# Performance work log

Measured on AMD Instinct MI355X. Metric: run time of the kernel, lower is better.

The kernel has to match this reference:

```python
import jax, jax.numpy as jnp
import numpy as np

NUM_HEADS = 12
EPS = 1e-6


def rms_norm(x, w):
    # torch nn.RMSNorm: x / sqrt(mean(x^2) + eps) * w, over last dim
    var = jnp.mean(jnp.square(x), axis=-1, keepdims=True)
    return x * jax.lax.rsqrt(var + EPS) * w


def rope2d_freqs(H, W, head_dim, dtype=jnp.float32):
    dim_x = head_dim // 2
    dim_y = head_dim - dim_x
    inv_freq_x = 1.0 / (10000.0 ** (jnp.arange(0, dim_x, 2, dtype=dtype) / dim_x))  # [dim_x//2]
    inv_freq_y = 1.0 / (10000.0 ** (jnp.arange(0, dim_y, 2, dtype=dtype) / dim_y))
    seq_x = jnp.arange(W, dtype=dtype)
    seq_y = jnp.arange(H, dtype=dtype)
    freqs_x = seq_x[:, None] * inv_freq_x[None, :]            # [W, dim_x//2]
    freqs_y = seq_y[:, None] * inv_freq_y[None, :]            # [H, dim_y//2]
    emb_x = jnp.concatenate([freqs_x, freqs_x], axis=-1)      # [W, dim_x]
    emb_y = jnp.concatenate([freqs_y, freqs_y], axis=-1)      # [H, dim_y]
    emb_x = jnp.broadcast_to(emb_x[None, :, :], (H, W, dim_x))
    emb_y = jnp.broadcast_to(emb_y[:, None, :], (H, W, dim_y))
    freqs = jnp.concatenate([emb_x, emb_y], axis=-1).reshape(H * W, head_dim)
    return freqs[None, :, :]  # [1, H*W, head_dim]


def rotate_half(x):
    x1, x2 = jnp.split(x, 2, axis=-1)
    return jnp.concatenate([-x2, x1], axis=-1)


def apply_rope(q, k, freqs):
    cos = jnp.cos(freqs)
    sin = jnp.sin(freqs)
    return q * cos + rotate_half(q) * sin, k * cos + rotate_half(k) * sin


def setup_inputs() -> dict:
    key = jax.random.key(0)
    ks = jax.random.split(key, 4)
    B, H, W, C = 16, 32, 32, 768
    N = 1 + H * W
    x = jax.random.normal(ks[0], (B, N, C), dtype=jnp.float32)
    qkv_w = jax.random.normal(ks[1], (C, 3 * C), dtype=jnp.float32) * (C ** -0.5)
    proj_w = jax.random.normal(ks[2], (C, C), dtype=jnp.float32) * (C ** -0.5)
    proj_b = jax.random.normal(ks[3], (C,), dtype=jnp.float32) * 0.01
    q_norm_w = jnp.ones((C // NUM_HEADS,), dtype=jnp.float32)
    k_norm_w = jnp.ones((C // NUM_HEADS,), dtype=jnp.float32)
    return {"x": x, "qkv_w": qkv_w, "proj_w": proj_w, "proj_b": proj_b,
            "q_norm_w": q_norm_w, "k_norm_w": k_norm_w, "H": H, "W": W}


def reference(x, qkv_w, proj_w, proj_b, q_norm_w, k_norm_w, H, W):
    B, N, C = x.shape
    h = NUM_HEADS
    d = C // h
    qkv = (x @ qkv_w).reshape(B, N, 3, h, d)
    qkv = jnp.transpose(qkv, (2, 0, 3, 1, 4))  # [3, B, h, N, d]
    q, k, v = qkv[0], qkv[1], qkv[2]
    q = rms_norm(q, q_norm_w)
    k = rms_norm(k, k_norm_w)
    cls_q, q = q[:, :, :1], q[:, :, 1:]
    cls_k, k = k[:, :, :1], k[:, :, 1:]
    freqs = rope2d_freqs(H, W, d, dtype=x.dtype)  # [1, H*W, d]
    q, k = apply_rope(q, k, freqs)
    q = jnp.concatenate([cls_q, q], axis=2)
    k = jnp.concatenate([cls_k, k], axis=2)
    scale = d ** -0.5
    scores = jnp.einsum('bhqd,bhkd->bhqk', q, k) * scale
    attn = jax.nn.softmax(scores, axis=-1)
    out = jnp.einsum('bhqk,bhkd->bhqd', attn, v)  # [B, h, N, d]
    out = jnp.transpose(out, (0, 2, 1, 3)).reshape(B, N, C)
    return out @ proj_w + proj_b
```

## Files before the change

kernel.cpp:

```cpp
#include <hip/hip_runtime.h>
#include <math.h>

#define NHEADS 12
#define HD 64
#define BB 16
#define NN 1025
#define CC 768
#define MM (BB * NN)
#define QSZ ((size_t)BB * NHEADS * NN * HD)
#define NNP 1032
#define VTSZ ((size_t)BB * NHEADS * HD * NNP)

typedef __attribute__((ext_vector_type(8))) short short8;
typedef __attribute__((ext_vector_type(4))) float f32x4;
typedef __attribute__((ext_vector_type(4))) unsigned short us4;
typedef __attribute__((ext_vector_type(4))) unsigned int u32x4;
typedef unsigned short us;

typedef __attribute__((address_space(3))) unsigned int lds_u32;
typedef const __attribute__((address_space(1))) unsigned int g_u32;

__device__ __forceinline__ void gload16(const void* g, void* l) {
    __builtin_amdgcn_global_load_lds((g_u32*)g, (lds_u32*)l, 16, 0, 0);
}

__device__ __forceinline__ int imin(int a, int b) { return a < b ? a : b; }

__device__ __forceinline__ us f2h(float f) {
    _Float16 h = (_Float16)f;
    return __builtin_bit_cast(unsigned short, h);
}
__device__ __forceinline__ float h2f(us b) {
    return (float)__builtin_bit_cast(_Float16, b);
}
__device__ __forceinline__ unsigned pkrtz(float a, float b) {
    return __builtin_bit_cast(unsigned, __builtin_amdgcn_cvt_pkrtz(a, b));
}

__global__ __launch_bounds__(256) void split_x(const float* __restrict__ src,
                                               us* __restrict__ xc) {
    size_t e = ((size_t)blockIdx.x * 256 + threadIdx.x) * 8;
    float4 a = *(const float4*)(src + e);
    float4 b = *(const float4*)(src + e + 4);
    float v[8] = {a.x, a.y, a.z, a.w, b.x, b.y, b.z, b.w};
    short8 h;
#pragma unroll
    for (int j = 0; j < 8; ++j) h[j] = (short)f2h(v[j]);
    *(short8*)(xc + e) = h;
}

__global__ __launch_bounds__(256) void tsplit(const float* __restrict__ w,
                                              us* __restrict__ wc, int N) {
    __shared__ float tile[64][65];
    const int t = threadIdx.x;
    const int n0 = blockIdx.x * 64, k0 = blockIdx.y * 64;
    {
        int kr = t & 63, so = t >> 6;
#pragma unroll
        for (int g = 0; g < 4; ++g) {
            int c = (so * 4 + g) * 4;
            float4 v = *(const float4*)(w + (size_t)(k0 + kr) * N + n0 + c);
            tile[kr][c + 0] = v.x; tile[kr][c + 1] = v.y;
            tile[kr][c + 2] = v.z; tile[kr][c + 3] = v.w;
        }
    }
    __syncthreads();
    int nr = t & 63, half = t >> 6;
    short8 h0, h1;
#pragma unroll
    for (int j = 0; j < 8; ++j) h0[j] = (short)f2h(tile[half * 16 + j][nr]);
#pragma unroll
    for (int j = 0; j < 8; ++j) h1[j] = (short)f2h(tile[half * 16 + 8 + j][nr]);
    size_t o = (size_t)(n0 + nr) * CC + k0 + half * 16;
    *(short8*)(wc + o)     = h0;
    *(short8*)(wc + o + 8) = h1;
}

template<int MODE>
__global__ __launch_bounds__(512) void gemm_mfma(
    const us* __restrict__ A,
    const us* __restrict__ B,
    us* __restrict__ Q, us* __restrict__ K, us* __restrict__ Vth,
    const float* __restrict__ qnw, const float* __restrict__ knw,
    float* __restrict__ fout, const float* __restrict__ bias) {
    __shared__ __align__(16) char lds[49152];
    char* ldsA = lds;
    char* ldsB = lds + 16384;
    const int tid = threadIdx.x;
    const int lane = tid & 63, wv = tid >> 6;
    const int wn = wv >> 2, wm = wv & 3;
    const int g = lane >> 4;

    const int gx = gridDim.x;
    const int nwg = gx * gridDim.y;
    const int lin = blockIdx.y * gx + blockIdx.x;
    const int qq = nwg >> 3, rr = nwg & 7;
    const int xcd = lin & 7, idx = lin >> 3;
    const int wgid = (xcd < rr ? xcd * (qq + 1) : rr * (qq + 1) + (xcd - rr) * qq) + idx;
    const int n0 = (wgid % gx) * 128, m0 = (wgid / gx) * 256;

    f32x4 acc[4][4];
    const f32x4 fz = {0.f, 0.f, 0.f, 0.f};
#pragma unroll
    for (int a = 0; a < 4; ++a)
#pragma unroll
        for (int b = 0; b < 4; ++b) acc[a][b] = fz;

    const int srow = (wv << 3) + (lane >> 3);
    const int cb   = (lane & 7) ^ ((lane >> 3) & 7);
    size_t aoff[2], boff[4];
#pragma unroll
    for (int i = 0; i < 2; ++i)
        aoff[i] = (size_t)(n0 + i * 64 + srow) * CC + cb * 8;
#pragma unroll
    for (int i = 0; i < 4; ++i)
        boff[i] = (size_t)imin(m0 + i * 64 + srow, MM - 1) * CC + cb * 8;
    const int wdst = wv * 1024;

    for (int t = 0; t < CC / 64; ++t) {
#pragma unroll
        for (int i = 0; i < 2; ++i)
            gload16(A + aoff[i] + t * 64, ldsA + i * 8192 + wdst);
#pragma unroll
        for (int i = 0; i < 4; ++i)
            gload16(B + boff[i] + t * 64, ldsB + i * 8192 + wdst);
        __syncthreads();

        const int j  = lane >> 4;
        const int rl = lane & 15;
#pragma unroll
        for (int kh = 0; kh < 2; ++kh) {
            short8 af[4];
#pragma unroll
            for (int nc = 0; nc < 4; ++nc) {
                int ra = wn * 64 + nc * 16 + rl;
                af[nc] = *(const short8*)(ldsA + ra * 128 + ((((kh << 2) + j) ^ (ra & 7)) << 4));
            }
            __builtin_amdgcn_s_setprio(1);
#pragma unroll
            for (int mc = 0; mc < 4; ++mc) {
                int rb = wm * 64 + mc * 16 + rl;
                short8 bf = *(const short8*)(ldsB + rb * 128 + ((((kh << 2) + j) ^ (rb & 7)) << 4));
#pragma unroll
                for (int nc = 0; nc < 4; ++nc)
                    acc[nc][mc] = __builtin_amdgcn_mfma_f32_16x16x32_f16(af[nc], bf, acc[nc][mc], 0, 0, 0);
            }
            __builtin_amdgcn_s_setprio(0);
        }
        __syncthreads();
    }

    if (MODE == 0) {
        const int s = n0 / CC;
        if (s < 2) {
            float2* lut = (float2*)lds;
            {
                int pos = tid >> 4, jj = tid & 15;
                float ang = (float)pos * exp2f((float)jj * (-13.287712379549449f / 16.0f));
                lut[tid] = make_float2(cosf(ang), sinf(ang));
            }
            __syncthreads();
            const float* wvec = (s == 0) ? qnw : knw;
            float wr[4][4];
#pragma unroll
            for (int nc = 0; nc < 4; ++nc)
#pragma unroll
                for (int r = 0; r < 4; ++r) wr[nc][r] = wvec[nc * 16 + g * 4 + r];
            const float qscale = (s == 0) ? 0.125f * 1.4426950408889634f : 1.0f;
            const int head = (n0 - s * CC + wn * 64) >> 6;
            us* dst = (s == 0) ? Q : K;

#pragma unroll
            for (int mc = 0; mc < 4; ++mc) {
                int m = m0 + wm * 64 + mc * 16 + (lane & 15);
                if (m >= MM) continue;
                int b = m / NN, t = m - b * NN;
                float v[4][4];
#pragma unroll
                for (int nc = 0; nc < 4; ++nc)
#pragma unroll
                    for (int r = 0; r < 4; ++r) v[nc][r] = acc[nc][mc][r];
                float ss = 0.f;
#pragma unroll
                for (int nc = 0; nc < 4; ++nc)
#pragma unroll
                    for (int r = 0; r < 4; ++r) ss += v[nc][r] * v[nc][r];
                ss += __shfl_xor(ss, 16);
                ss += __shfl_xor(ss, 32);
                float rn = 1.0f / sqrtf(ss * (1.0f / 64.0f) + 1e-6f);
#pragma unroll
                for (int nc = 0; nc < 4; ++nc)
#pragma unroll
                    for (int r = 0; r < 4; ++r) v[nc][r] *= rn * wr[nc][r];
                if (t > 0) {
                    int px = (t - 1) & 31, py = (t - 1) >> 5;
#pragma unroll
                    for (int r = 0; r < 4; ++r) {
                        float2 ex = lut[px * 16 + g * 4 + r];
                        float2 ey = lut[py * 16 + g * 4 + r];
                        float n0v = v[0][r] * ex.x - v[2][r] * ex.y;
                        float n1v = v[1][r] * ex.x - v[3][r] * ex.y;
                        float n2v = v[2][r] * ey.x + v[0][r] * ey.y;
                        float n3v = v[3][r] * ey.x + v[1][r] * ey.y;
                        v[0][r] = n0v; v[1][r] = n1v; v[2][r] = n2v; v[3][r] = n3v;
                    }
                }
                int bh = b * NHEADS + head;
                size_t rbase = ((size_t)bh * NN + t) * HD;
#pragma unroll
                for (int nc = 0; nc < 4; ++nc) {
                    us4 h4;
#pragma unroll
                    for (int r = 0; r < 4; ++r) h4[r] = f2h(v[nc][r] * qscale);
                    *(us4*)(dst + rbase + nc * 16 + g * 4) = h4;
                }
            }
        } else {
#pragma unroll
            for (int mc = 0; mc < 4; ++mc) {
                int m = m0 + wm * 64 + mc * 16 + (lane & 15);
                if (m >= MM) continue;
                int b = m / NN, t = m - b * NN;
#pragma unroll
                for (int nc = 0; nc < 4; ++nc) {
                    int nin = (n0 - 2 * CC) + wn * 64 + nc * 16 + g * 4;
                    int head = nin >> 6;
                    int dd = nin & 63;
                    int bh = b * NHEADS + head;
#pragma unroll
                    for (int r = 0; r < 4; ++r) {
                        size_t idx2 = ((size_t)bh * HD + dd + r) * NNP + t;
                        Vth[idx2] = f2h(acc[nc][mc][r]);
                        if (t == NN - 1) {
#pragma unroll
                            for (int tt = 1; tt <= 7; ++tt) Vth[idx2 + tt] = 0;
                        }
                    }
                }
            }
        }
    } else {
#pragma unroll
        for (int mc = 0; mc < 4; ++mc) {
            int m = m0 + wm * 64 + mc * 16 + (lane & 15);
            if (m >= MM) continue;
#pragma unroll
            for (int nc = 0; nc < 4; ++nc) {
                int n = n0 + wn * 64 + nc * 16 + (g << 2);
                float4 o = {acc[nc][mc][0] + bias[n + 0], acc[nc][mc][1] + bias[n + 1],
                            acc[nc][mc][2] + bias[n + 2], acc[nc][mc][3] + bias[n + 3]};
                *(float4*)(fout + (size_t)m * CC + n) = o;
            }
        }
    }
}

__global__ __launch_bounds__(256, 4) void attn_mfma(
    const us* __restrict__ Q, const us* __restrict__ K,
    const us* __restrict__ Vth, us* __restrict__ OC) {
    __shared__ __align__(16) char smem[36864];
    const int tid = threadIdx.x;
    const int lane = tid & 63, wv = tid >> 6;
    const int g = lane >> 4, qi = lane & 15;

    int lin = blockIdx.x;
    int xcd = lin & 7, loc = lin >> 3;
    int bh  = (loc / 9) * 8 + xcd;
    int qb  = loc - (loc / 9) * 9;
    const int q0 = qb * 128;

    const size_t kbase0 = (size_t)bh * NN * HD;
    const size_t vbase0 = (size_t)bh * HD * NNP;

    short8 qf[2][2];
#pragma unroll
    for (int h = 0; h < 2; ++h) {
        int qr = imin(q0 + (wv << 5) + (h << 4) + qi, NN - 1);
        const us* qp = Q + kbase0 + (size_t)qr * HD + (g << 3);
        qf[h][0] = *(const short8*)(qp);
        qf[h][1] = *(const short8*)(qp + 32);
    }

    f32x4 oa[2][5];
    const f32x4 fz = {0.f, 0.f, 0.f, 0.f};
#pragma unroll
    for (int h = 0; h < 2; ++h)
#pragma unroll
        for (int db = 0; db < 5; ++db) oa[h][db] = fz;

    const int VB = 8192;

    *(uint2*)(smem + VB + 8192 + tid * 8) = (uint2){0x3C003C00u, 0x3C003C00u};
    *(uint2*)(smem + 18432 + VB + 8192 + tid * 8) = (uint2){0x3C003C00u, 0x3C003C00u};

    int rbase[2];
#pragma unroll
    for (int ks = 0; ks < 2; ++ks)
        rbase[ks] = qi * 128 + (((ks << 6) + (g << 4)) ^ ((qi & 7) << 4));

    const int srow = (wv << 4) + (lane >> 3);
    const int sg   = lane & 7;
    int kwoff[2], vwoff[2];
#pragma unroll
    for (int i = 0; i < 2; ++i) {
        int row = srow + (i << 3);
        int pp = ((row >> 5) << 5) | (((row >> 2) & 1) << 4) |
                 (((row >> 3) & 3) << 2) | (row & 3);
        kwoff[i] = pp * 128 + ((sg << 4) ^ ((pp & 7) << 4));
        vwoff[i] = VB + row * 128 + ((sg << 4) ^ ((row & 7) << 4));
    }

    const us* kp = K   + kbase0 + (size_t)srow * HD  + (sg << 3);
    const us* vp = Vth + vbase0 + (size_t)srow * NNP + (sg << 3);
    short8 pkh[2], pvh[2];
    pkh[0] = *(const short8*)kp;
    pkh[1] = *(const short8*)(kp + 8 * HD);
    pvh[0] = *(const short8*)vp;
    pvh[1] = *(const short8*)(vp + 8 * NNP);
    kp += 64 * HD; vp += 64;

    auto step = [&](int t, char* buf) {
        *(short8*)(buf + kwoff[0]) = pkh[0];
        *(short8*)(buf + kwoff[1]) = pkh[1];
        *(short8*)(buf + vwoff[0]) = pvh[0];
        *(short8*)(buf + vwoff[1]) = pvh[1];
        __syncthreads();
        if (t < 16) {
            pkh[0] = *(const short8*)kp;
            pkh[1] = *(const short8*)(kp + 8 * HD);
            pvh[0] = *(const short8*)vp;
            pvh[1] = *(const short8*)(vp + 8 * NNP);
            kp += 64 * HD; vp += 64;
        }
        const int j0 = t * 64;

        short8 pa[2][2];
#pragma unroll
        for (int h = 0; h < 2; ++h) {
            f32x4 sc[4];
#pragma unroll
            for (int c = 0; c < 4; ++c) sc[c] = fz;
            __builtin_amdgcn_s_setprio(1);
#pragma unroll
            for (int ks = 0; ks < 2; ++ks)
#pragma unroll
                for (int c = 0; c < 4; ++c) {
                    short8 kfh = *(const short8*)(buf + rbase[ks] + c * 2048);
                    sc[c] = __builtin_amdgcn_mfma_f32_16x16x32_f16(kfh, qf[h][ks], sc[c], 0, 0, 0);
                }
            __builtin_amdgcn_s_setprio(0);

            if (j0 + 64 > NN) {
#pragma unroll
                for (int c = 0; c < 4; ++c)
#pragma unroll
                    for (int r = 0; r < 4; ++r)
                        if (j0 + ((c >> 1) << 5) + (g << 3) + ((c & 1) << 2) + r >= NN)
                            sc[c][r] = -1e30f;
            }
#pragma unroll
            for (int ks = 0; ks < 2; ++ks) {
                u32x4 w;
                w[0] = pkrtz(exp2f(sc[2 * ks][0]), exp2f(sc[2 * ks][1]));
                w[1] = pkrtz(exp2f(sc[2 * ks][2]), exp2f(sc[2 * ks][3]));
                w[2] = pkrtz(exp2f(sc[2 * ks + 1][0]), exp2f(sc[2 * ks + 1][1]));
                w[3] = pkrtz(exp2f(sc[2 * ks + 1][2]), exp2f(sc[2 * ks + 1][3]));
                pa[h][ks] = __builtin_bit_cast(short8, w);
            }
        }

        __builtin_amdgcn_s_setprio(1);
#pragma unroll
        for (int ks = 0; ks < 2; ++ks)
#pragma unroll
            for (int db = 0; db < 5; ++db) {
                short8 vfh = *(const short8*)(buf + VB + rbase[ks] + db * 2048);
                oa[0][db] = __builtin_amdgcn_mfma_f32_16x16x32_f16(pa[0][ks], vfh, oa[0][db], 0, 0, 0);
                oa[1][db] = __builtin_amdgcn_mfma_f32_16x16x32_f16(pa[1][ks], vfh, oa[1][db], 0, 0, 0);
            }
        __builtin_amdgcn_s_setprio(0);
    };

#pragma unroll 1
    for (int tt = 0; tt < 8; ++tt) {
        step(2 * tt,     smem);
        step(2 * tt + 1, smem + 18432);
    }
    step(16, smem);

    const int b = bh / NHEADS, hh = bh - b * NHEADS;
#pragma unroll
    for (int h = 0; h < 2; ++h)
#pragma unroll
        for (int r = 0; r < 4; ++r) {
            int q = q0 + (wv << 5) + (h << 4) + (g << 2) + r;
            float linv = 1.0f / oa[h][4][r];
            if (q < NN) {
#pragma unroll
                for (int db = 0; db < 4; ++db) {
                    int d = (db << 4) + qi;
                    OC[(size_t)(b * NN + q) * CC + hh * HD + d] = f2h(oa[h][db][r] * linv);
                }
            }
        }
}

extern "C" void kernel_launch(void* const* d_in, const int* in_sizes, int n_in,
                              void* d_out, int out_size, void* d_ws, size_t ws_size,
                              hipStream_t stream) {
    const float* x      = (const float*)d_in[0];
    const float* qkv_w  = (const float*)d_in[1];
    const float* proj_w = (const float*)d_in[2];
    const float* proj_b = (const float*)d_in[3];
    const float* qnw    = (const float*)d_in[4];
    const float* knw    = (const float*)d_in[5];

    us* p = (us*)d_ws;
    us* Q   = p;                 p += QSZ;
    us* K   = p;                 p += QSZ;
    us* Vth = p;                 p += VTSZ;
    us* XC  = p;                 p += (size_t)MM * CC;
    us* WC  = p;                 p += (size_t)3 * CC * CC;
    us* PC  = p;                 p += (size_t)CC * CC;

    split_x<<<dim3((int)(((size_t)MM * CC) / 8 / 256)), 256, 0, stream>>>(x, XC);
    tsplit<<<dim3(3 * CC / 64, CC / 64), 256, 0, stream>>>(qkv_w, WC, 3 * CC);
    tsplit<<<dim3(CC / 64, CC / 64), 256, 0, stream>>>(proj_w, PC, CC);

    gemm_mfma<0><<<dim3(18, (MM + 255) / 256), 512, 0, stream>>>(
        WC, XC, Q, K, Vth, qnw, knw, nullptr, nullptr);
    attn_mfma<<<dim3(8 * 216), 256, 0, stream>>>(Q, K, Vth, XC);
    gemm_mfma<1><<<dim3(6, (MM + 255) / 256), 512, 0, stream>>>(
        PC, XC, nullptr, nullptr, nullptr, nullptr, nullptr,
        (float*)d_out, proj_b);
}
```

Baseline: 224.4 us.

## Stage attention K/V tiles via direct global-to-LDS loads with source-side swizzle

The attention kernel stops prefetching K/V tiles into registers and writing them to LDS. It now issues global_load_lds 16-byte loads straight into the next double buffer, and permutes the global source addresses so the LDS layout keeps the existing swizzled read pattern. The QK^T MFMAs for both query halves are interleaved so each loaded K fragment is used twice. The barrier moves to the end of each step, and the launch-bounds occupancy hint of 4 is dropped. The aim is to save VGPRs and LDS-store instructions and to overlap the copy with compute. The risks are correct wait-count handling before the barrier and a different register and occupancy outcome.

Measured after the change: 228.3 us. Within noise of the previous version (+1.7%).

```diff
diff --git a/kernel.cpp b/kernel.cpp
--- a/kernel.cpp
+++ b/kernel.cpp
@@ -255,7 +255,7 @@
     }
 }
 
-__global__ __launch_bounds__(256, 4) void attn_mfma(
+__global__ __launch_bounds__(256) void attn_mfma(
     const us* __restrict__ Q, const us* __restrict__ K,
     const us* __restrict__ Vth, us* __restrict__ OC) {
     __shared__ __align__(16) char smem[36864];
@@ -289,85 +289,85 @@
         for (int db = 0; db < 5; ++db) oa[h][db] = fz;
 
     const int VB = 8192;
+    const int BUFS = 18432;
 
     *(uint2*)(smem + VB + 8192 + tid * 8) = (uint2){0x3C003C00u, 0x3C003C00u};
-    *(uint2*)(smem + 18432 + VB + 8192 + tid * 8) = (uint2){0x3C003C00u, 0x3C003C00u};
+    *(uint2*)(smem + BUFS + VB + 8192 + tid * 8) = (uint2){0x3C003C00u, 0x3C003C00u};
 
     int rbase[2];
 #pragma unroll
     for (int ks = 0; ks < 2; ++ks)
         rbase[ks] = qi * 128 + (((ks << 6) + (g << 4)) ^ ((qi & 7) << 4));
 
-    const int srow = (wv << 4) + (lane >> 3);
-    const int sg   = lane & 7;
-    int kwoff[2], vwoff[2];
+    const int lrow = lane >> 3, lslot = lane & 7;
+    const us* ks_[2];
+    const us* vs_[2];
 #pragma unroll
     for (int i = 0; i < 2; ++i) {
-        int row = srow + (i << 3);
-        int pp = ((row >> 5) << 5) | (((row >> 2) & 1) << 4) |
-                 (((row >> 3) & 3) << 2) | (row & 3);
-        kwoff[i] = pp * 128 + ((sg << 4) ^ ((pp & 7) << 4));
-        vwoff[i] = VB + row * 128 + ((sg << 4) ^ ((row & 7) << 4));
-    }
-
-    const us* kp = K   + kbase0 + (size_t)srow * HD  + (sg << 3);
-    const us* vp = Vth + vbase0 + (size_t)srow * NNP + (sg << 3);
-    short8 pkh[2], pvh[2];
-    pkh[0] = *(const short8*)kp;
-    pkh[1] = *(const short8*)(kp + 8 * HD);
-    pvh[0] = *(const short8*)vp;
-    pvh[1] = *(const short8*)(vp + 8 * NNP);
-    kp += 64 * HD; vp += 64;
-
-    auto step = [&](int t, char* buf) {
-        *(short8*)(buf + kwoff[0]) = pkh[0];
-        *(short8*)(buf + kwoff[1]) = pkh[1];
-        *(short8*)(buf + vwoff[0]) = pvh[0];
-        *(short8*)(buf + vwoff[1]) = pvh[1];
-        __syncthreads();
-        if (t < 16) {
-            pkh[0] = *(const short8*)kp;
-            pkh[1] = *(const short8*)(kp + 8 * HD);
-            pvh[0] = *(const short8*)vp;
-            pvh[1] = *(const short8*)(vp + 8 * NNP);
-            kp += 64 * HD; vp += 64;
+        int pp  = (wv << 4) + (i << 3) + lrow;
+        int sig = ((pp >> 5) << 5) | (((pp >> 3) & 1) << 4) |
+                  (((pp >> 2) & 1) << 3) | (((pp >> 4) & 1) << 2) | (pp & 3);
+        ks_[i] = K + kbase0 + (size_t)sig * HD + ((lslot ^ (pp & 7)) << 3);
+        vs_[i] = Vth + vbase0 + (size_t)pp * NNP + ((lslot ^ lrow) << 3);
+    }
+    const int kd0 = wv * 2048, kd1 = wv * 2048 + 1024;
+
+    gload16(ks_[0], smem + kd0);
+    gload16(ks_[1], smem + kd1);
+    gload16(vs_[0], smem + VB + kd0);
+    gload16(vs_[1], smem + VB + kd1);
+    ks_[0] += 64 * HD; ks_[1] += 64 * HD; vs_[0] += 64; vs_[1] += 64;
+    __syncthreads();
+
+    auto step = [&](int t, char* buf, char* bufn, bool stage) {
+        if (stage) {
+            gload16(ks_[0], bufn + kd0);
+            gload16(ks_[1], bufn + kd1);
+            gload16(vs_[0], bufn + VB + kd0);
+            gload16(vs_[1], bufn + VB + kd1);
+            ks_[0] += 64 * HD; ks_[1] += 64 * HD; vs_[0] += 64; vs_[1] += 64;
         }
         const int j0 = t * 64;
 
+        f32x4 sc[2][4];
+#pragma unroll
+        for (int h = 0; h < 2; ++h)
+#pragma unroll
+            for (int c = 0; c < 4; ++c) sc[h][c] = fz;
+        __builtin_amdgcn_s_setprio(1);
+#pragma unroll
+        for (int ks = 0; ks < 2; ++ks)
+#pragma unroll
+            for (int c = 0; c < 4; ++c) {
+                short8 kfh = *(const short8*)(buf + rbase[ks] + c * 2048);
+                sc[0][c] = __builtin_amdgcn_mfma_f32_16x16x32_f16(kfh, qf[0][ks], sc[0][c], 0, 0, 0);
+                sc[1][c] = __builtin_amdgcn_mfma_f32_16x16x32_f16(kfh, qf[1][ks], sc[1][c], 0, 0, 0);
+            }
+        __builtin_amdgcn_s_setprio(0);
+
+        if (j0 + 64 > NN) {
+#pragma unroll
+            for (int c = 0; c < 4; ++c)
+#pragma unroll
+                for (int r = 0; r < 4; ++r)
+                    if (j0 + ((c >> 1) << 5) + (g << 3) + ((c & 1) << 2) + r >= NN) {
+                        sc[0][c][r] = -1e30f;
+                        sc[1][c][r] = -1e30f;
+                    }
+        }
+
         short8 pa[2][2];
 #pragma unroll
-        for (int h = 0; h < 2; ++h) {
-            f32x4 sc[4];
-#pragma unroll
-            for (int c = 0; c < 4; ++c) sc[c] = fz;
-            __builtin_amdgcn_s_setprio(1);
-#pragma unroll
-            for (int ks = 0; ks < 2; ++ks)
-#pragma unroll
-                for (int c = 0; c < 4; ++c) {
-                    short8 kfh = *(const short8*)(buf + rbase[ks] + c * 2048);
-                    sc[c] = __builtin_amdgcn_mfma_f32_16x16x32_f16(kfh, qf[h][ks], sc[c], 0, 0, 0);
-                }
-            __builtin_amdgcn_s_setprio(0);
-
-            if (j0 + 64 > NN) {
-#pragma unroll
-                for (int c = 0; c < 4; ++c)
-#pragma unroll
-                    for (int r = 0; r < 4; ++r)
-                        if (j0 + ((c >> 1) << 5) + (g << 3) + ((c & 1) << 2) + r >= NN)
-                            sc[c][r] = -1e30f;
-            }
+        for (int h = 0; h < 2; ++h)
 #pragma unroll
             for (int ks = 0; ks < 2; ++ks) {
                 u32x4 w;
-                w[0] = pkrtz(exp2f(sc[2 * ks][0]), exp2f(sc[2 * ks][1]));
-                w[1] = pkrtz(exp2f(sc[2 * ks][2]), exp2f(sc[2 * ks][3]));
-                w[2] = pkrtz(exp2f(sc[2 * ks + 1][0]), exp2f(sc[2 * ks + 1][1]));
-                w[3] = pkrtz(exp2f(sc[2 * ks + 1][2]), exp2f(sc[2 * ks + 1][3]));
+                w[0] = pkrtz(exp2f(sc[h][2 * ks][0]), exp2f(sc[h][2 * ks][1]));
+                w[1] = pkrtz(exp2f(sc[h][2 * ks][2]), exp2f(sc[h][2 * ks][3]));
+                w[2] = pkrtz(exp2f(sc[h][2 * ks + 1][0]), exp2f(sc[h][2 * ks + 1][1]));
+                w[3] = pkrtz(exp2f(sc[h][2 * ks + 1][2]), exp2f(sc[h][2 * ks + 1][3]));
                 pa[h][ks] = __builtin_bit_cast(short8, w);
             }
-        }
 
         __builtin_amdgcn_s_setprio(1);
 #pragma unroll
@@ -379,14 +379,15 @@
                 oa[1][db] = __builtin_amdgcn_mfma_f32_16x16x32_f16(pa[1][ks], vfh, oa[1][db], 0, 0, 0);
             }
         __builtin_amdgcn_s_setprio(0);
+        __syncthreads();
     };
 
 #pragma unroll 1
     for (int tt = 0; tt < 8; ++tt) {
-        step(2 * tt,     smem);
-        step(2 * tt + 1, smem + 18432);
-    }
-    step(16, smem);
+        step(2 * tt,     smem,        smem + BUFS, true);
+        step(2 * tt + 1, smem + BUFS, smem,        true);
+    }
+    step(16, smem, smem + BUFS, false);
 
     const int b = bh / NHEADS, hh = bh - b * NHEADS;
 #pragma unroll
```
